# Kernel optimization log

Hardware: AMD Instinct MI355X
Metric: run time of the kernel (lower is better)

## Reference

```python
import jax, jax.numpy as jnp
import numpy as np

NUM_NODES = 5  # the 5 ASPP branches form the graph nodes


def conv2d(x, w, b, padding=0, dilation=1):
    # NCHW conv with OIHW kernel, stride 1
    out = jax.lax.conv_general_dilated(
        x, w, window_strides=(1, 1),
        padding=[(padding, padding), (padding, padding)],
        rhs_dilation=(dilation, dilation),
        dimension_numbers=("NCHW", "OIHW", "NCHW"))
    return out + b[None, :, None, None]


def setup_inputs() -> dict:
    key = jax.random.key(0)
    ks = jax.random.split(key, 16)
    Cin, Cmid, Cout = 32, 16, 32
    B, H, W = 8, 384, 384
    s = 0.05
    inp = {
        "x": jax.random.normal(ks[0], (B, Cin, H, W), jnp.float32),
        "w1": jax.random.normal(ks[1], (Cmid, Cin, 1, 1), jnp.float32) * s,
        "b1": jax.random.normal(ks[2], (Cmid,), jnp.float32) * s,
        "w2": jax.random.normal(ks[3], (Cmid, Cin, 3, 3), jnp.float32) * s,
        "b2": jax.random.normal(ks[4], (Cmid,), jnp.float32) * s,
        "w3": jax.random.normal(ks[5], (Cmid, Cin, 3, 3), jnp.float32) * s,
        "b3": jax.random.normal(ks[6], (Cmid,), jnp.float32) * s,
        "w4": jax.random.normal(ks[7], (Cmid, Cin, 3, 3), jnp.float32) * s,
        "b4": jax.random.normal(ks[8], (Cmid,), jnp.float32) * s,
        "w5": jax.random.normal(ks[9], (Cmid, Cin, 1, 1), jnp.float32) * s,
        "b5": jax.random.normal(ks[10], (Cmid,), jnp.float32) * s,
        "gcn_w": jax.random.normal(ks[11], (Cmid, Cmid), jnp.float32) * s,
        "gcn_b": jax.random.normal(ks[12], (Cmid,), jnp.float32) * s,
        "attn_weights": jnp.ones((NUM_NODES,), jnp.float32),
        "fusion_w": jax.random.normal(ks[13], (Cout, Cmid, 1, 1), jnp.float32) * s,
        "fusion_b": jax.random.normal(ks[14], (Cout,), jnp.float32) * s,
    }
    return inp


def reference(x, w1, b1, w2, b2, w3, b3, w4, b4, w5, b5,
              gcn_w, gcn_b, attn_weights, fusion_w, fusion_b):
    # --- ASPP branches ---
    f1 = conv2d(x, w1, b1)                     # 1x1
    f2 = conv2d(x, w2, b2, padding=1, dilation=1)
    f3 = conv2d(x, w3, b3, padding=2, dilation=2)
    f4 = conv2d(x, w4, b4, padding=3, dilation=3)
    gap = x.mean(axis=(2, 3), keepdims=True)   # AdaptiveAvgPool2d(1)
    f5 = conv2d(gap, w5, b5)                   # [B, mid, 1, 1]
    # bilinear upsample of a 1x1 map (align_corners=False) == broadcast
    f5 = jnp.broadcast_to(f5, f1.shape)
    feats = jnp.stack([f1, f2, f3, f4, f5], axis=1)  # [B, 5, mid, H, W]

    # --- node features: per-branch global mean ---
    node_feats = feats.mean(axis=(3, 4))       # [B, 5, mid]

    # --- GCNConv on complete 5-node graph (self-loops added by GCNConv):
    # A_hat = D^{-1/2}(A+I)D^{-1/2} = ones(5,5)/5. Batched over samples.
    A_hat = jnp.full((NUM_NODES, NUM_NODES), 1.0 / NUM_NODES, dtype=x.dtype)
    fused_nodes = jnp.einsum("ij,bjc->bic", A_hat, node_feats @ gcn_w) + gcn_b  # [B,5,mid]

    # --- weighted node fusion ---
    weights = jax.nn.softmax(attn_weights)     # [5]
    out = jnp.einsum("i,bichw,bic->bchw", weights, feats, fused_nodes)  # [B, mid, H, W]

    return conv2d(out, fusion_w, fusion_b)     # [B, out, H, W]
```

## Files before the change

kernel.cpp:

```cpp
#include <hip/hip_runtime.h>
#include <math.h>

#define HH 384
#define WW 384
#define BB 8
#define CIN 32
#define CMID 16
#define COUT 32
#define HWP (HH*WW)

#define WS_GAP  0
#define WS_BORD 256
#define WS_F5   12544
#define WS_CB   12672
#define WS_W2   12928
#define WS_WBF  17024
#define WS_S    32768

typedef __attribute__((ext_vector_type(8))) __bf16 bf16x8;
typedef __attribute__((ext_vector_type(4))) float  f32x4;

__device__ __forceinline__ unsigned bf16r(float f) {
    unsigned u = __float_as_uint(f);
    return (u + 0x7fffu + ((u >> 16) & 1u)) >> 16;
}

__device__ __forceinline__ void softmax5(const float* attn, float sw[5]) {
    float a0=attn[0],a1=attn[1],a2=attn[2],a3=attn[3],a4=attn[4];
    float m = fmaxf(fmaxf(fmaxf(a0,a1),fmaxf(a2,a3)),a4);
    float e0=expf(a0-m),e1=expf(a1-m),e2=expf(a2-m),e3=expf(a3-m),e4=expf(a4-m);
    float inv = 1.f/(e0+e1+e2+e3+e4);
    sw[0]=e0*inv; sw[1]=e1*inv; sw[2]=e2*inv; sw[3]=e3*inv; sw[4]=e4*inv;
}

__global__ void gap_kernel(const float* __restrict__ x, float* __restrict__ gap) {
    int plane = blockIdx.x;
    const float4* xp = (const float4*)(x + (size_t)plane * HWP);
    float s = 0.f;
    for (int i = threadIdx.x; i < HWP/4; i += 1024) {
        float4 v = xp[i];
        s += (v.x + v.y) + (v.z + v.w);
    }
    __shared__ float red[16];
    #pragma unroll
    for (int o = 32; o; o >>= 1) s += __shfl_down(s, o);
    if ((threadIdx.x & 63) == 0) red[threadIdx.x >> 6] = s;
    __syncthreads();
    if (threadIdx.x < 16) {
        float t = red[threadIdx.x];
        #pragma unroll
        for (int o = 8; o; o >>= 1) t += __shfl_down(t, o);
        if (threadIdx.x == 0) gap[plane] = t * (1.f / (float)HWP);
    }
}

__device__ __forceinline__ float blockReduce256(float v, float* red) {
    #pragma unroll
    for (int o = 32; o; o >>= 1) v += __shfl_down(v, o);
    if ((threadIdx.x & 63) == 0) red[threadIdx.x >> 6] = v;
    __syncthreads();
    float r = 0.f;
    if (threadIdx.x == 0) r = red[0] + red[1] + red[2] + red[3];
    __syncthreads();
    return r;
}

__global__ void border_kernel(const float* __restrict__ x, float* __restrict__ bord) {
    int plane = blockIdx.x;
    const float* xp = x + (size_t)plane * HWP;
    __shared__ float red[4];
    __shared__ float rs[6], cs[6];
    int t = threadIdx.x;
    for (int j = 0; j < 6; ++j) {
        int r = (j < 3) ? j : 378 + j;
        float s = 0.f;
        for (int i = t; i < WW; i += 256) s += xp[r*WW + i];
        s = blockReduce256(s, red);
        if (t == 0) rs[j] = s;
    }
    for (int j = 0; j < 6; ++j) {
        int c = (j < 3) ? j : 378 + j;
        float s = 0.f;
        for (int i = t; i < HH; i += 256) s += xp[i*WW + c];
        s = blockReduce256(s, red);
        if (t == 0) cs[j] = s;
    }
    __syncthreads();
    if (t == 0) {
        float* bd = bord + plane*48;
        bd[0]=rs[0]; bd[1]=rs[0]+rs[1]; bd[2]=rs[0]+rs[1]+rs[2];
        bd[3]=rs[5]; bd[4]=rs[5]+rs[4]; bd[5]=rs[5]+rs[4]+rs[3];
        bd[6]=cs[0]; bd[7]=cs[0]+cs[1]; bd[8]=cs[0]+cs[1]+cs[2];
        bd[9]=cs[5]; bd[10]=cs[5]+cs[4]; bd[11]=cs[5]+cs[4]+cs[3];
        for (int a = 1; a <= 3; ++a)
        for (int b2 = 1; b2 <= 3; ++b2) {
            float tl=0,tr=0,bl=0,br=0;
            for (int h = 0; h < a; ++h)
            for (int w = 0; w < b2; ++w) {
                tl += xp[h*WW + w];
                tr += xp[h*WW + (WW-1-w)];
                bl += xp[(HH-1-h)*WW + w];
                br += xp[(HH-1-h)*WW + (WW-1-w)];
            }
            int o = (a-1)*3 + (b2-1);
            bd[12+o]=tl; bd[21+o]=tr; bd[30+o]=bl; bd[39+o]=br;
        }
    }
}

__global__ void prep1_kernel(const float* __restrict__ w1, const float* __restrict__ w2,
                             const float* __restrict__ w3, const float* __restrict__ w4,
                             const float* __restrict__ w5, const float* __restrict__ b5,
                             const float* __restrict__ attn, float* __restrict__ ws) {
    const float* gap = ws + WS_GAP;
    float* f5 = ws + WS_F5;
    unsigned short* wbf = (unsigned short*)(ws + WS_WBF);
    float sw[5];
    softmax5(attn, sw);
    int t = threadIdx.x;
    if (t < 128) {
        int b = t >> 4, c = t & 15;
        float acc = b5[c];
        for (int ci = 0; ci < CIN; ++ci) acc += w5[c*CIN+ci] * gap[b*CIN+ci];
        f5[t] = acc;
    }
    const int tk[8] = {0,1,2,3,5,6,7,8};
    for (int idx = t; idx < 25*512; idx += blockDim.x) {
        int tap  = idx >> 9;
        int lane = (idx >> 3) & 63;
        int j    = idx & 7;
        int cin  = ((lane >> 4) << 3) | j;
        int c    = lane & 15;
        float v;
        if (tap == 0) {
            v = sw[0]*w1[c*CIN+cin]
              + sw[1]*w2[c*288 + cin*9 + 4]
              + sw[2]*w3[c*288 + cin*9 + 4]
              + sw[3]*w4[c*288 + cin*9 + 4];
        } else {
            int g = (tap-1) >> 3;
            int m = (tap-1) & 7;
            int kk = tk[m];
            const float* w = (g == 0) ? w2 : ((g == 1) ? w3 : w4);
            v = sw[g+1] * w[c*288 + cin*9 + kk];
        }
        wbf[idx] = (unsigned short)bf16r(v);
    }
}

__global__ __launch_bounds__(256) void conv_kernel(
        const float* __restrict__ x, const unsigned short* __restrict__ wBf,
        float* __restrict__ S) {
    __shared__ __align__(16) unsigned short sx[484*40];
    int blk = blockIdx.x;
    int b = blk / 576; int tno = blk % 576;
    int h0 = (tno / 24) * 16, w0 = (tno % 24) * 16;
    int tid = threadIdx.x;

    int i0 = tid, i1 = tid + 256;
    int r0i = i0 / 22, c0i = i0 - r0i*22;
    int r1i = i1 / 22, c1i = i1 - r1i*22;
    int gh0 = h0 - 3 + r0i, gw0 = w0 - 3 + c0i;
    int gh1 = h0 - 3 + r1i, gw1 = w0 - 3 + c1i;
    bool ok0 = ((unsigned)gh0 < (unsigned)HH) && ((unsigned)gw0 < (unsigned)WW);
    bool ok1 = ((unsigned)gh1 < (unsigned)HH) && ((unsigned)gw1 < (unsigned)WW) && (i1 < 484);
    bool has1 = (i1 < 484);
    int go0 = ok0 ? (gh0*WW + gw0) : 0;
    int go1 = ok1 ? (gh1*WW + gw1) : 0;
    unsigned* sxu = (unsigned*)sx;
    const float* xb = x + (size_t)b * CIN * HWP;
    #pragma unroll 4
    for (int cp = 0; cp < 16; ++cp) {
        const float* p0 = xb + (size_t)(2*cp) * HWP;
        const float* p1 = p0 + HWP;
        float a0 = ok0 ? p0[go0] : 0.f;
        float a1 = ok0 ? p1[go0] : 0.f;
        sxu[i0*20 + cp] = bf16r(a0) | (bf16r(a1) << 16);
        if (has1) {
            float d0 = ok1 ? p0[go1] : 0.f;
            float d1 = ok1 ? p1[go1] : 0.f;
            sxu[i1*20 + cp] = bf16r(d0) | (bf16r(d1) << 16);
        }
    }
    __syncthreads();

    int lane = tid & 63, wv = tid >> 6;
    int m = lane & 15, q = lane >> 4;
    int by0 = ((wv*4 + 0 + 3)*22 + 3 + m)*40 + q*8;
    int by1 = by0 + 22*40;
    int by2 = by1 + 22*40;
    int by3 = by2 + 22*40;
    const unsigned short* wfp = wBf + lane*8;

    f32x4 acc0 = {0.f,0.f,0.f,0.f}, acc1 = {0.f,0.f,0.f,0.f};
    f32x4 acc2 = {0.f,0.f,0.f,0.f}, acc3 = {0.f,0.f,0.f,0.f};

    constexpr int TDH[25] = {0, -1,-1,-1,0,0,1,1,1, -2,-2,-2,0,0,2,2,2, -3,-3,-3,0,0,3,3,3};
    constexpr int TDW[25] = {0, -1,0,1,-1,1,-1,0,1, -2,0,2,-2,2,-2,0,2, -3,0,3,-3,3,-3,0,3};
    #pragma unroll
    for (int tap = 0; tap < 25; ++tap) {
        bf16x8 bw = *(const bf16x8*)(wfp + tap*512);
        const int to = (TDH[tap]*22 + TDW[tap])*40;
        acc0 = __builtin_amdgcn_mfma_f32_16x16x32_bf16(*(const bf16x8*)(sx + by0 + to), bw, acc0, 0, 0, 0);
        acc1 = __builtin_amdgcn_mfma_f32_16x16x32_bf16(*(const bf16x8*)(sx + by1 + to), bw, acc1, 0, 0, 0);
        acc2 = __builtin_amdgcn_mfma_f32_16x16x32_bf16(*(const bf16x8*)(sx + by2 + to), bw, acc2, 0, 0, 0);
        acc3 = __builtin_amdgcn_mfma_f32_16x16x32_bf16(*(const bf16x8*)(sx + by3 + to), bw, acc3, 0, 0, 0);
    }

    #pragma unroll
    for (int g2 = 0; g2 < 4; ++g2) {
        int y = wv*4 + g2;
        float* sp = S + ((size_t)b*HWP + (size_t)(h0 + y)*WW + w0) * 16;
        f32x4 a = (g2 == 0) ? acc0 : (g2 == 1) ? acc1 : (g2 == 2) ? acc2 : acc3;
        #pragma unroll
        for (int r = 0; r < 4; ++r) {
            int px = q*4 + r;
            sp[px*16 + m] = a[r];
        }
    }
}

__device__ __forceinline__ float rectsum(const float* bd, float T, int dh, int dw) {
    int r0 = dh > 0 ?  dh : 0, b0 = dh < 0 ? -dh : 0;
    int c0 = dw > 0 ?  dw : 0, d0 = dw < 0 ? -dw : 0;
    float v = T;
    if (r0) v -= bd[r0-1];
    if (b0) v -= bd[3+b0-1];
    if (c0) v -= bd[6+c0-1];
    if (d0) v -= bd[9+d0-1];
    if (r0 && c0) v += bd[12+(r0-1)*3+(c0-1)];
    if (r0 && d0) v += bd[21+(r0-1)*3+(d0-1)];
    if (b0 && c0) v += bd[30+(b0-1)*3+(c0-1)];
    if (b0 && d0) v += bd[39+(b0-1)*3+(d0-1)];
    return v;
}

__global__ void prep2_kernel(const float* __restrict__ w1,
                             const float* __restrict__ b1, const float* __restrict__ w2,
                             const float* __restrict__ b2, const float* __restrict__ w3,
                             const float* __restrict__ b3, const float* __restrict__ w4,
                             const float* __restrict__ b4,
                             const float* __restrict__ gcn_w, const float* __restrict__ gcn_b,
                             const float* __restrict__ fusion_w, const float* __restrict__ fusion_b,
                             const float* __restrict__ attn, float* __restrict__ ws) {
    const float* gap  = ws + WS_GAP;
    const float* bord = ws + WS_BORD;
    const float* f5   = ws + WS_F5;
    float* W2 = ws + WS_W2;
    float* CB = ws + WS_CB;
    __shared__ float ns[128];
    __shared__ float bbf[128];
    __shared__ float gl[128];
    float sw[5];
    softmax5(attn, sw);
    int t = threadIdx.x;
    const float invHW = 1.f / (float)HWP;
    if (t < 128) {
        int b = t >> 4, c = t & 15;
        float nf1 = b1[c];
        float s2 = 0.f, s3 = 0.f, s4 = 0.f;
        for (int cin = 0; cin < CIN; ++cin) {
            nf1 += w1[c*CIN+cin] * gap[b*CIN+cin];
            const float* bd = bord + (b*CIN + cin)*48;
            float T = gap[b*CIN+cin] * (float)HWP;
            #pragma unroll
            for (int kk = 0; kk < 9; ++kk) {
                int dh = (kk/3) - 1, dw = (kk%3) - 1;
                float wv2 = w2[c*288 + cin*9 + kk];
                float wv3 = w3[c*288 + cin*9 + kk];
                float wv4 = w4[c*288 + cin*9 + kk];
                s2 += wv2 * rectsum(bd, T, dh,   dw);
                s3 += wv3 * rectsum(bd, T, 2*dh, 2*dw);
                s4 += wv4 * rectsum(bd, T, 3*dh, 3*dw);
            }
        }
        float nf2 = b2[c] + s2*invHW;
        float nf3 = b3[c] + s3*invHW;
        float nf4 = b4[c] + s4*invHW;
        float nf5 = f5[b*16 + c];
        ns[t]  = 0.2f * (nf1 + nf2 + nf3 + nf4 + nf5);
        bbf[t] = sw[0]*b1[c] + sw[1]*b2[c] + sw[2]*b3[c] + sw[3]*b4[c] + sw[4]*nf5;
    }
    __syncthreads();
    if (t < 128) {
        int b = t >> 4, c = t & 15;
        float acc = gcn_b[c];
        for (int k = 0; k < 16; ++k) acc += ns[b*16 + k] * gcn_w[k*16 + c];
        gl[t] = acc;
    }
    __syncthreads();
    for (int idx = t; idx < 4096; idx += blockDim.x) {
        int b = idx >> 9, c = (idx >> 5) & 15, co = idx & 31;
        W2[idx] = fusion_w[co*16 + c] * gl[b*16 + c];
    }
    if (t < 256) {
        int b = t >> 5, co = t & 31;
        float acc = fusion_b[co];
        for (int c = 0; c < 16; ++c)
            acc += fusion_w[co*16 + c] * gl[b*16 + c] * bbf[b*16 + c];
        CB[t] = acc;
    }
}

__global__ __launch_bounds__(256) void fuse_kernel(const float* __restrict__ ws_ro,
                                                   float* __restrict__ out) {
    __shared__ float w2s[512];
    __shared__ float cbs[32];
    int blk = blockIdx.x;
    int b = blk / 576;
    int pl = (blk % 576) * 256 + threadIdx.x;
    int t = threadIdx.x;
    const float* W2 = ws_ro + WS_W2 + b*512;
    w2s[t] = W2[t];
    w2s[t + 256] = W2[t + 256];
    if (t < 32) cbs[t] = ws_ro[WS_CB + b*32 + t];
    __syncthreads();

    const float4* sp = (const float4*)(ws_ro + WS_S + ((size_t)b*HWP + pl)*16);
    float4 s0 = sp[0], s1 = sp[1], s2 = sp[2], s3 = sp[3];
    float sv[16] = {s0.x,s0.y,s0.z,s0.w, s1.x,s1.y,s1.z,s1.w,
                    s2.x,s2.y,s2.z,s2.w, s3.x,s3.y,s3.z,s3.w};
    float acc[32];
    #pragma unroll
    for (int co = 0; co < 32; ++co) acc[co] = cbs[co];
    #pragma unroll
    for (int c = 0; c < 16; ++c) {
        float v = sv[c];
        #pragma unroll
        for (int co = 0; co < 32; ++co) acc[co] = fmaf(w2s[c*32 + co], v, acc[co]);
    }
    float* ob = out + (size_t)b * COUT * HWP + pl;
    #pragma unroll
    for (int co = 0; co < 32; ++co) ob[(size_t)co * HWP] = acc[co];
}

extern "C" void kernel_launch(void* const* d_in, const int* in_sizes, int n_in,
                              void* d_out, int out_size, void* d_ws, size_t ws_size,
                              hipStream_t stream) {
    const float* x     = (const float*)d_in[0];
    const float* w1    = (const float*)d_in[1];  const float* b1 = (const float*)d_in[2];
    const float* w2    = (const float*)d_in[3];  const float* b2 = (const float*)d_in[4];
    const float* w3    = (const float*)d_in[5];  const float* b3 = (const float*)d_in[6];
    const float* w4    = (const float*)d_in[7];  const float* b4 = (const float*)d_in[8];
    const float* w5    = (const float*)d_in[9];  const float* b5 = (const float*)d_in[10];
    const float* gcn_w = (const float*)d_in[11]; const float* gcn_b = (const float*)d_in[12];
    const float* attn  = (const float*)d_in[13];
    const float* fw    = (const float*)d_in[14]; const float* fb = (const float*)d_in[15];
    float* ws  = (float*)d_ws;
    float* out = (float*)d_out;

    gap_kernel   <<<256, 1024, 0, stream>>>(x, ws + WS_GAP);
    border_kernel<<<256, 256, 0, stream>>>(x, ws + WS_BORD);
    prep1_kernel <<<1, 256, 0, stream>>>(w1, w2, w3, w4, w5, b5, attn, ws);
    conv_kernel  <<<4608, 256, 0, stream>>>(x, (const unsigned short*)(ws + WS_WBF), ws + WS_S);
    prep2_kernel <<<1, 256, 0, stream>>>(w1, b1, w2, b2, w3, b3, w4, b4,
                                         gcn_w, gcn_b, fw, fb, attn, ws);
    fuse_kernel  <<<4608, 256, 0, stream>>>(ws, out);
}
```

Before: 485.1 us.

## Fuse conv and fusion stages, precompute NHWC bf16 input with fused reductions

Adds a transform pass that reads x once, writes a channel-last bf16 copy, and in the same pass accumulates global sums and border row/column sums with atomics. This replaces the separate gap and border kernels. The conv kernel now loads contiguous bf16 pixel vectors, and the per-pixel 16→32 fusion projection is fused into it through shared memory, so the fp32 intermediate S buffer is never written or read back. The added cost is an extra write and read of a bf16 copy of x, plus atomics and a memset.

```diff
diff --git a/kernel.cpp b/kernel.cpp
--- a/kernel.cpp
+++ b/kernel.cpp
@@ -3,19 +3,16 @@
 
 #define HH 384
 #define WW 384
-#define BB 8
 #define CIN 32
-#define CMID 16
-#define COUT 32
 #define HWP (HH*WW)
 
-#define WS_GAP  0
-#define WS_BORD 256
-#define WS_F5   12544
-#define WS_CB   12672
-#define WS_W2   12928
-#define WS_WBF  17024
-#define WS_S    32768
+#define WS_GSUM 0
+#define WS_ROWS 256
+#define WS_COLS 1792
+#define WS_W2   3328
+#define WS_CB   7424
+#define WS_WBF  7680
+#define WS_XBF  16384
 
 typedef __attribute__((ext_vector_type(8))) __bf16 bf16x8;
 typedef __attribute__((ext_vector_type(4))) float  f32x4;
@@ -33,190 +30,46 @@
     sw[0]=e0*inv; sw[1]=e1*inv; sw[2]=e2*inv; sw[3]=e3*inv; sw[4]=e4*inv;
 }
 
-__global__ void gap_kernel(const float* __restrict__ x, float* __restrict__ gap) {
-    int plane = blockIdx.x;
-    const float4* xp = (const float4*)(x + (size_t)plane * HWP);
-    float s = 0.f;
-    for (int i = threadIdx.x; i < HWP/4; i += 1024) {
-        float4 v = xp[i];
-        s += (v.x + v.y) + (v.z + v.w);
-    }
-    __shared__ float red[16];
-    #pragma unroll
-    for (int o = 32; o; o >>= 1) s += __shfl_down(s, o);
-    if ((threadIdx.x & 63) == 0) red[threadIdx.x >> 6] = s;
-    __syncthreads();
-    if (threadIdx.x < 16) {
-        float t = red[threadIdx.x];
+__global__ __launch_bounds__(384) void transform_kernel(const float* __restrict__ x,
+        float* __restrict__ ws, unsigned short* __restrict__ xbf) {
+    int b = blockIdx.x / HH, h = blockIdx.x % HH;
+    int t = threadIdx.x;
+    const float* xp = x + (size_t)b*CIN*HWP + (size_t)h*WW + t;
+    float v[32];
+    #pragma unroll
+    for (int ci = 0; ci < 32; ++ci) v[ci] = xp[(size_t)ci*HWP];
+
+    unsigned uu[16];
+    #pragma unroll
+    for (int k = 0; k < 16; ++k) uu[k] = bf16r(v[2*k]) | (bf16r(v[2*k+1]) << 16);
+    uint4* dst = (uint4*)(xbf + ((size_t)b*HWP + (size_t)h*WW + t)*32);
+    dst[0] = make_uint4(uu[0],uu[1],uu[2],uu[3]);
+    dst[1] = make_uint4(uu[4],uu[5],uu[6],uu[7]);
+    dst[2] = make_uint4(uu[8],uu[9],uu[10],uu[11]);
+    dst[3] = make_uint4(uu[12],uu[13],uu[14],uu[15]);
+
+    int cj = (t < 3) ? t : ((t >= 381) ? t - 378 : -1);
+    if (cj >= 0) {
         #pragma unroll
-        for (int o = 8; o; o >>= 1) t += __shfl_down(t, o);
-        if (threadIdx.x == 0) gap[plane] = t * (1.f / (float)HWP);
-    }
-}
-
-__device__ __forceinline__ float blockReduce256(float v, float* red) {
-    #pragma unroll
-    for (int o = 32; o; o >>= 1) v += __shfl_down(v, o);
-    if ((threadIdx.x & 63) == 0) red[threadIdx.x >> 6] = v;
-    __syncthreads();
-    float r = 0.f;
-    if (threadIdx.x == 0) r = red[0] + red[1] + red[2] + red[3];
-    __syncthreads();
-    return r;
-}
-
-__global__ void border_kernel(const float* __restrict__ x, float* __restrict__ bord) {
-    int plane = blockIdx.x;
-    const float* xp = x + (size_t)plane * HWP;
-    __shared__ float red[4];
-    __shared__ float rs[6], cs[6];
-    int t = threadIdx.x;
-    for (int j = 0; j < 6; ++j) {
-        int r = (j < 3) ? j : 378 + j;
-        float s = 0.f;
-        for (int i = t; i < WW; i += 256) s += xp[r*WW + i];
-        s = blockReduce256(s, red);
-        if (t == 0) rs[j] = s;
-    }
-    for (int j = 0; j < 6; ++j) {
-        int c = (j < 3) ? j : 378 + j;
-        float s = 0.f;
-        for (int i = t; i < HH; i += 256) s += xp[i*WW + c];
-        s = blockReduce256(s, red);
-        if (t == 0) cs[j] = s;
-    }
-    __syncthreads();
-    if (t == 0) {
-        float* bd = bord + plane*48;
-        bd[0]=rs[0]; bd[1]=rs[0]+rs[1]; bd[2]=rs[0]+rs[1]+rs[2];
-        bd[3]=rs[5]; bd[4]=rs[5]+rs[4]; bd[5]=rs[5]+rs[4]+rs[3];
-        bd[6]=cs[0]; bd[7]=cs[0]+cs[1]; bd[8]=cs[0]+cs[1]+cs[2];
-        bd[9]=cs[5]; bd[10]=cs[5]+cs[4]; bd[11]=cs[5]+cs[4]+cs[3];
-        for (int a = 1; a <= 3; ++a)
-        for (int b2 = 1; b2 <= 3; ++b2) {
-            float tl=0,tr=0,bl=0,br=0;
-            for (int h = 0; h < a; ++h)
-            for (int w = 0; w < b2; ++w) {
-                tl += xp[h*WW + w];
-                tr += xp[h*WW + (WW-1-w)];
-                bl += xp[(HH-1-h)*WW + w];
-                br += xp[(HH-1-h)*WW + (WW-1-w)];
-            }
-            int o = (a-1)*3 + (b2-1);
-            bd[12+o]=tl; bd[21+o]=tr; bd[30+o]=bl; bd[39+o]=br;
-        }
-    }
-}
-
-__global__ void prep1_kernel(const float* __restrict__ w1, const float* __restrict__ w2,
-                             const float* __restrict__ w3, const float* __restrict__ w4,
-                             const float* __restrict__ w5, const float* __restrict__ b5,
-                             const float* __restrict__ attn, float* __restrict__ ws) {
-    const float* gap = ws + WS_GAP;
-    float* f5 = ws + WS_F5;
-    unsigned short* wbf = (unsigned short*)(ws + WS_WBF);
-    float sw[5];
-    softmax5(attn, sw);
-    int t = threadIdx.x;
-    if (t < 128) {
-        int b = t >> 4, c = t & 15;
-        float acc = b5[c];
-        for (int ci = 0; ci < CIN; ++ci) acc += w5[c*CIN+ci] * gap[b*CIN+ci];
-        f5[t] = acc;
-    }
-    const int tk[8] = {0,1,2,3,5,6,7,8};
-    for (int idx = t; idx < 25*512; idx += blockDim.x) {
-        int tap  = idx >> 9;
-        int lane = (idx >> 3) & 63;
-        int j    = idx & 7;
-        int cin  = ((lane >> 4) << 3) | j;
-        int c    = lane & 15;
-        float v;
-        if (tap == 0) {
-            v = sw[0]*w1[c*CIN+cin]
-              + sw[1]*w2[c*288 + cin*9 + 4]
-              + sw[2]*w3[c*288 + cin*9 + 4]
-              + sw[3]*w4[c*288 + cin*9 + 4];
-        } else {
-            int g = (tap-1) >> 3;
-            int m = (tap-1) & 7;
-            int kk = tk[m];
-            const float* w = (g == 0) ? w2 : ((g == 1) ? w3 : w4);
-            v = sw[g+1] * w[c*288 + cin*9 + kk];
-        }
-        wbf[idx] = (unsigned short)bf16r(v);
-    }
-}
-
-__global__ __launch_bounds__(256) void conv_kernel(
-        const float* __restrict__ x, const unsigned short* __restrict__ wBf,
-        float* __restrict__ S) {
-    __shared__ __align__(16) unsigned short sx[484*40];
-    int blk = blockIdx.x;
-    int b = blk / 576; int tno = blk % 576;
-    int h0 = (tno / 24) * 16, w0 = (tno % 24) * 16;
-    int tid = threadIdx.x;
-
-    int i0 = tid, i1 = tid + 256;
-    int r0i = i0 / 22, c0i = i0 - r0i*22;
-    int r1i = i1 / 22, c1i = i1 - r1i*22;
-    int gh0 = h0 - 3 + r0i, gw0 = w0 - 3 + c0i;
-    int gh1 = h0 - 3 + r1i, gw1 = w0 - 3 + c1i;
-    bool ok0 = ((unsigned)gh0 < (unsigned)HH) && ((unsigned)gw0 < (unsigned)WW);
-    bool ok1 = ((unsigned)gh1 < (unsigned)HH) && ((unsigned)gw1 < (unsigned)WW) && (i1 < 484);
-    bool has1 = (i1 < 484);
-    int go0 = ok0 ? (gh0*WW + gw0) : 0;
-    int go1 = ok1 ? (gh1*WW + gw1) : 0;
-    unsigned* sxu = (unsigned*)sx;
-    const float* xb = x + (size_t)b * CIN * HWP;
-    #pragma unroll 4
-    for (int cp = 0; cp < 16; ++cp) {
-        const float* p0 = xb + (size_t)(2*cp) * HWP;
-        const float* p1 = p0 + HWP;
-        float a0 = ok0 ? p0[go0] : 0.f;
-        float a1 = ok0 ? p1[go0] : 0.f;
-        sxu[i0*20 + cp] = bf16r(a0) | (bf16r(a1) << 16);
-        if (has1) {
-            float d0 = ok1 ? p0[go1] : 0.f;
-            float d1 = ok1 ? p1[go1] : 0.f;
-            sxu[i1*20 + cp] = bf16r(d0) | (bf16r(d1) << 16);
-        }
-    }
-    __syncthreads();
-
-    int lane = tid & 63, wv = tid >> 6;
-    int m = lane & 15, q = lane >> 4;
-    int by0 = ((wv*4 + 0 + 3)*22 + 3 + m)*40 + q*8;
-    int by1 = by0 + 22*40;
-    int by2 = by1 + 22*40;
-    int by3 = by2 + 22*40;
-    const unsigned short* wfp = wBf + lane*8;
-
-    f32x4 acc0 = {0.f,0.f,0.f,0.f}, acc1 = {0.f,0.f,0.f,0.f};
-    f32x4 acc2 = {0.f,0.f,0.f,0.f}, acc3 = {0.f,0.f,0.f,0.f};
-
-    constexpr int TDH[25] = {0, -1,-1,-1,0,0,1,1,1, -2,-2,-2,0,0,2,2,2, -3,-3,-3,0,0,3,3,3};
-    constexpr int TDW[25] = {0, -1,0,1,-1,1,-1,0,1, -2,0,2,-2,2,-2,0,2, -3,0,3,-3,3,-3,0,3};
-    #pragma unroll
-    for (int tap = 0; tap < 25; ++tap) {
-        bf16x8 bw = *(const bf16x8*)(wfp + tap*512);
-        const int to = (TDH[tap]*22 + TDW[tap])*40;
-        acc0 = __builtin_amdgcn_mfma_f32_16x16x32_bf16(*(const bf16x8*)(sx + by0 + to), bw, acc0, 0, 0, 0);
-        acc1 = __builtin_amdgcn_mfma_f32_16x16x32_bf16(*(const bf16x8*)(sx + by1 + to), bw, acc1, 0, 0, 0);
-        acc2 = __builtin_amdgcn_mfma_f32_16x16x32_bf16(*(const bf16x8*)(sx + by2 + to), bw, acc2, 0, 0, 0);
-        acc3 = __builtin_amdgcn_mfma_f32_16x16x32_bf16(*(const bf16x8*)(sx + by3 + to), bw, acc3, 0, 0, 0);
-    }
-
-    #pragma unroll
-    for (int g2 = 0; g2 < 4; ++g2) {
-        int y = wv*4 + g2;
-        float* sp = S + ((size_t)b*HWP + (size_t)(h0 + y)*WW + w0) * 16;
-        f32x4 a = (g2 == 0) ? acc0 : (g2 == 1) ? acc1 : (g2 == 2) ? acc2 : acc3;
+        for (int ci = 0; ci < 32; ++ci)
+            atomicAdd(&ws[WS_COLS + (b*32 + ci)*6 + cj], v[ci]);
+    }
+
+    __shared__ float red[32][6];
+    int wv = t >> 6, ln = t & 63;
+    #pragma unroll
+    for (int ci = 0; ci < 32; ++ci) {
+        float s = v[ci];
         #pragma unroll
-        for (int r = 0; r < 4; ++r) {
-            int px = q*4 + r;
-            sp[px*16 + m] = a[r];
-        }
+        for (int o = 32; o; o >>= 1) s += __shfl_down(s, o);
+        if (ln == 0) red[ci][wv] = s;
+    }
+    __syncthreads();
+    if (t < 32) {
+        float rsum = red[t][0]+red[t][1]+red[t][2]+red[t][3]+red[t][4]+red[t][5];
+        atomicAdd(&ws[WS_GSUM + b*32 + t], rsum);
+        int rj = (h < 3) ? h : ((h >= 381) ? h - 378 : -1);
+        if (rj >= 0) ws[WS_ROWS + (b*32 + t)*6 + rj] = rsum;
     }
 }
 
@@ -235,51 +88,103 @@
     return v;
 }
 
-__global__ void prep2_kernel(const float* __restrict__ w1,
-                             const float* __restrict__ b1, const float* __restrict__ w2,
-                             const float* __restrict__ b2, const float* __restrict__ w3,
-                             const float* __restrict__ b3, const float* __restrict__ w4,
-                             const float* __restrict__ b4,
-                             const float* __restrict__ gcn_w, const float* __restrict__ gcn_b,
-                             const float* __restrict__ fusion_w, const float* __restrict__ fusion_b,
-                             const float* __restrict__ attn, float* __restrict__ ws) {
-    const float* gap  = ws + WS_GAP;
-    const float* bord = ws + WS_BORD;
-    const float* f5   = ws + WS_F5;
-    float* W2 = ws + WS_W2;
-    float* CB = ws + WS_CB;
-    __shared__ float ns[128];
-    __shared__ float bbf[128];
-    __shared__ float gl[128];
+__global__ void prep_kernel(const float* __restrict__ x,
+                            const float* __restrict__ w1, const float* __restrict__ b1,
+                            const float* __restrict__ w2, const float* __restrict__ b2,
+                            const float* __restrict__ w3, const float* __restrict__ b3,
+                            const float* __restrict__ w4, const float* __restrict__ b4,
+                            const float* __restrict__ w5, const float* __restrict__ b5,
+                            const float* __restrict__ gcn_w, const float* __restrict__ gcn_b,
+                            const float* __restrict__ fusion_w, const float* __restrict__ fusion_b,
+                            const float* __restrict__ attn, float* __restrict__ ws) {
+    __shared__ float sbd[256*48];
+    __shared__ float ns[128], bbf[128], gl[128];
     float sw[5];
     softmax5(attn, sw);
     int t = threadIdx.x;
     const float invHW = 1.f / (float)HWP;
+
+    {
+        int plane = t;
+        float* bd = sbd + plane*48;
+        const float* rw = ws + WS_ROWS + plane*6;
+        const float* cl = ws + WS_COLS + plane*6;
+        bd[0]=rw[0]; bd[1]=rw[0]+rw[1]; bd[2]=rw[0]+rw[1]+rw[2];
+        bd[3]=rw[5]; bd[4]=rw[5]+rw[4]; bd[5]=rw[5]+rw[4]+rw[3];
+        bd[6]=cl[0]; bd[7]=cl[0]+cl[1]; bd[8]=cl[0]+cl[1]+cl[2];
+        bd[9]=cl[5]; bd[10]=cl[5]+cl[4]; bd[11]=cl[5]+cl[4]+cl[3];
+        const float* xp = x + (size_t)plane*HWP;
+        for (int a = 1; a <= 3; ++a)
+        for (int b2 = 1; b2 <= 3; ++b2) {
+            float tl=0,tr=0,bl=0,br=0;
+            for (int h = 0; h < a; ++h)
+            for (int w = 0; w < b2; ++w) {
+                tl += xp[h*WW + w];
+                tr += xp[h*WW + (WW-1-w)];
+                bl += xp[(HH-1-h)*WW + w];
+                br += xp[(HH-1-h)*WW + (WW-1-w)];
+            }
+            int o = (a-1)*3 + (b2-1);
+            bd[12+o]=tl; bd[21+o]=tr; bd[30+o]=bl; bd[39+o]=br;
+        }
+    }
+
+    float f5v = 0.f;
+    if (t < 128) {
+        int b = t >> 4, c = t & 15;
+        f5v = b5[c];
+        for (int ci = 0; ci < CIN; ++ci)
+            f5v += w5[c*CIN+ci] * ws[WS_GSUM + b*32 + ci] * invHW;
+    }
+    {
+        unsigned short* wbf = (unsigned short*)(ws + WS_WBF);
+        const int tk[8] = {0,1,2,3,5,6,7,8};
+        for (int idx = t; idx < 25*512; idx += blockDim.x) {
+            int tap  = idx >> 9;
+            int lane = (idx >> 3) & 63;
+            int j    = idx & 7;
+            int cin  = ((lane >> 4) << 3) | j;
+            int c    = lane & 15;
+            float v;
+            if (tap == 0) {
+                v = sw[0]*w1[c*CIN+cin]
+                  + sw[1]*w2[c*288 + cin*9 + 4]
+                  + sw[2]*w3[c*288 + cin*9 + 4]
+                  + sw[3]*w4[c*288 + cin*9 + 4];
+            } else {
+                int g = (tap-1) >> 3;
+                int mth = (tap-1) & 7;
+                int kk = tk[mth];
+                const float* w = (g == 0) ? w2 : ((g == 1) ? w3 : w4);
+                v = sw[g+1] * w[c*288 + cin*9 + kk];
+            }
+            wbf[idx] = (unsigned short)bf16r(v);
+        }
+    }
+    __syncthreads();
+
     if (t < 128) {
         int b = t >> 4, c = t & 15;
         float nf1 = b1[c];
         float s2 = 0.f, s3 = 0.f, s4 = 0.f;
         for (int cin = 0; cin < CIN; ++cin) {
-            nf1 += w1[c*CIN+cin] * gap[b*CIN+cin];
-            const float* bd = bord + (b*CIN + cin)*48;
-            float T = gap[b*CIN+cin] * (float)HWP;
+            int plane = b*32 + cin;
+            float T = ws[WS_GSUM + plane];
+            nf1 += w1[c*CIN+cin] * T * invHW;
+            const float* bd = sbd + plane*48;
             #pragma unroll
             for (int kk = 0; kk < 9; ++kk) {
                 int dh = (kk/3) - 1, dw = (kk%3) - 1;
-                float wv2 = w2[c*288 + cin*9 + kk];
-                float wv3 = w3[c*288 + cin*9 + kk];
-                float wv4 = w4[c*288 + cin*9 + kk];
-                s2 += wv2 * rectsum(bd, T, dh,   dw);
-                s3 += wv3 * rectsum(bd, T, 2*dh, 2*dw);
-                s4 += wv4 * rectsum(bd, T, 3*dh, 3*dw);
+                s2 += w2[c*288 + cin*9 + kk] * rectsum(bd, T, dh,   dw);
+                s3 += w3[c*288 + cin*9 + kk] * rectsum(bd, T, 2*dh, 2*dw);
+                s4 += w4[c*288 + cin*9 + kk] * rectsum(bd, T, 3*dh, 3*dw);
             }
         }
         float nf2 = b2[c] + s2*invHW;
         float nf3 = b3[c] + s3*invHW;
         float nf4 = b4[c] + s4*invHW;
-        float nf5 = f5[b*16 + c];
-        ns[t]  = 0.2f * (nf1 + nf2 + nf3 + nf4 + nf5);
-        bbf[t] = sw[0]*b1[c] + sw[1]*b2[c] + sw[2]*b3[c] + sw[3]*b4[c] + sw[4]*nf5;
+        ns[t]  = 0.2f * (nf1 + nf2 + nf3 + nf4 + f5v);
+        bbf[t] = sw[0]*b1[c] + sw[1]*b2[c] + sw[2]*b3[c] + sw[3]*b4[c] + sw[4]*f5v;
     }
     __syncthreads();
     if (t < 128) {
@@ -291,35 +196,86 @@
     __syncthreads();
     for (int idx = t; idx < 4096; idx += blockDim.x) {
         int b = idx >> 9, c = (idx >> 5) & 15, co = idx & 31;
-        W2[idx] = fusion_w[co*16 + c] * gl[b*16 + c];
-    }
-    if (t < 256) {
+        ws[WS_W2 + idx] = fusion_w[co*16 + c] * gl[b*16 + c];
+    }
+    {
         int b = t >> 5, co = t & 31;
         float acc = fusion_b[co];
         for (int c = 0; c < 16; ++c)
             acc += fusion_w[co*16 + c] * gl[b*16 + c] * bbf[b*16 + c];
-        CB[t] = acc;
-    }
-}
-
-__global__ __launch_bounds__(256) void fuse_kernel(const float* __restrict__ ws_ro,
-                                                   float* __restrict__ out) {
-    __shared__ float w2s[512];
-    __shared__ float cbs[32];
+        ws[WS_CB + t] = acc;
+    }
+}
+
+__global__ __launch_bounds__(256) void convfuse_kernel(
+        const unsigned short* __restrict__ xbf, const unsigned short* __restrict__ wBf,
+        const float* __restrict__ ws_ro, float* __restrict__ out) {
+    __shared__ __align__(16) char smem[40896];
+    unsigned short* sx = (unsigned short*)smem;
+    float* w2s = (float*)(smem + 38720);
+    float* cbs = (float*)(smem + 40768);
     int blk = blockIdx.x;
-    int b = blk / 576;
-    int pl = (blk % 576) * 256 + threadIdx.x;
-    int t = threadIdx.x;
-    const float* W2 = ws_ro + WS_W2 + b*512;
-    w2s[t] = W2[t];
-    w2s[t + 256] = W2[t + 256];
-    if (t < 32) cbs[t] = ws_ro[WS_CB + b*32 + t];
-    __syncthreads();
-
-    const float4* sp = (const float4*)(ws_ro + WS_S + ((size_t)b*HWP + pl)*16);
-    float4 s0 = sp[0], s1 = sp[1], s2 = sp[2], s3 = sp[3];
-    float sv[16] = {s0.x,s0.y,s0.z,s0.w, s1.x,s1.y,s1.z,s1.w,
-                    s2.x,s2.y,s2.z,s2.w, s3.x,s3.y,s3.z,s3.w};
+    int b = blk / 576, tno = blk % 576;
+    int h0 = (tno / 24) * 16, w0 = (tno % 24) * 16;
+    int tid = threadIdx.x;
+
+    w2s[tid]       = ws_ro[WS_W2 + b*512 + tid];
+    w2s[tid + 256] = ws_ro[WS_W2 + b*512 + 256 + tid];
+    if (tid < 32) cbs[tid] = ws_ro[WS_CB + b*32 + tid];
+
+    for (int p = tid; p < 484; p += 256) {
+        int r = p / 22, c = p - r*22;
+        int gh = h0 - 3 + r, gw = w0 - 3 + c;
+        uint4 a0 = {0,0,0,0}, a1 = a0, a2 = a0, a3 = a0;
+        if ((unsigned)gh < (unsigned)HH && (unsigned)gw < (unsigned)WW) {
+            const uint4* src = (const uint4*)(xbf + ((size_t)b*HWP + (size_t)gh*WW + gw)*32);
+            a0 = src[0]; a1 = src[1]; a2 = src[2]; a3 = src[3];
+        }
+        uint4* d = (uint4*)(sx + p*40);
+        d[0] = a0; d[1] = a1; d[2] = a2; d[3] = a3;
+    }
+    __syncthreads();
+
+    int lane = tid & 63, wv = tid >> 6;
+    int m = lane & 15, q = lane >> 4;
+    int by0 = ((wv*4 + 0 + 3)*22 + 3 + m)*40 + q*8;
+    int by1 = by0 + 22*40;
+    int by2 = by1 + 22*40;
+    int by3 = by2 + 22*40;
+    const unsigned short* wfp = wBf + lane*8;
+
+    f32x4 acc0 = {0.f,0.f,0.f,0.f}, acc1 = {0.f,0.f,0.f,0.f};
+    f32x4 acc2 = {0.f,0.f,0.f,0.f}, acc3 = {0.f,0.f,0.f,0.f};
+
+    constexpr int TDH[25] = {0, -1,-1,-1,0,0,1,1,1, -2,-2,-2,0,0,2,2,2, -3,-3,-3,0,0,3,3,3};
+    constexpr int TDW[25] = {0, -1,0,1,-1,1,-1,0,1, -2,0,2,-2,2,-2,0,2, -3,0,3,-3,3,-3,0,3};
+    #pragma unroll
+    for (int tap = 0; tap < 25; ++tap) {
+        bf16x8 bw = *(const bf16x8*)(wfp + tap*512);
+        const int to = (TDH[tap]*22 + TDW[tap])*40;
+        acc0 = __builtin_amdgcn_mfma_f32_16x16x32_bf16(*(const bf16x8*)(sx + by0 + to), bw, acc0, 0, 0, 0);
+        acc1 = __builtin_amdgcn_mfma_f32_16x16x32_bf16(*(const bf16x8*)(sx + by1 + to), bw, acc1, 0, 0, 0);
+        acc2 = __builtin_amdgcn_mfma_f32_16x16x32_bf16(*(const bf16x8*)(sx + by2 + to), bw, acc2, 0, 0, 0);
+        acc3 = __builtin_amdgcn_mfma_f32_16x16x32_bf16(*(const bf16x8*)(sx + by3 + to), bw, acc3, 0, 0, 0);
+    }
+    __syncthreads();
+
+    float* st = (float*)smem;
+    #pragma unroll
+    for (int g2 = 0; g2 < 4; ++g2) {
+        int y = wv*4 + g2;
+        f32x4 a = (g2 == 0) ? acc0 : (g2 == 1) ? acc1 : (g2 == 2) ? acc2 : acc3;
+        #pragma unroll
+        for (int r = 0; r < 4; ++r) {
+            int px = q*4 + r;
+            st[(y*16 + px)*17 + m] = a[r];
+        }
+    }
+    __syncthreads();
+
+    float sv[16];
+    #pragma unroll
+    for (int c = 0; c < 16; ++c) sv[c] = st[tid*17 + c];
     float acc[32];
     #pragma unroll
     for (int co = 0; co < 32; ++co) acc[co] = cbs[co];
@@ -329,7 +285,8 @@
         #pragma unroll
         for (int co = 0; co < 32; ++co) acc[co] = fmaf(w2s[c*32 + co], v, acc[co]);
     }
-    float* ob = out + (size_t)b * COUT * HWP + pl;
+    int y = tid >> 4, px = tid & 15;
+    float* ob = out + (size_t)b*32*HWP + (size_t)(h0 + y)*WW + w0 + px;
     #pragma unroll
     for (int co = 0; co < 32; ++co) ob[(size_t)co * HWP] = acc[co];
 }
@@ -348,12 +305,11 @@
     const float* fw    = (const float*)d_in[14]; const float* fb = (const float*)d_in[15];
     float* ws  = (float*)d_ws;
     float* out = (float*)d_out;
-
-    gap_kernel   <<<256, 1024, 0, stream>>>(x, ws + WS_GAP);
-    border_kernel<<<256, 256, 0, stream>>>(x, ws + WS_BORD);
-    prep1_kernel <<<1, 256, 0, stream>>>(w1, w2, w3, w4, w5, b5, attn, ws);
-    conv_kernel  <<<4608, 256, 0, stream>>>(x, (const unsigned short*)(ws + WS_WBF), ws + WS_S);
-    prep2_kernel <<<1, 256, 0, stream>>>(w1, b1, w2, b2, w3, b3, w4, b4,
-                                         gcn_w, gcn_b, fw, fb, attn, ws);
-    fuse_kernel  <<<4608, 256, 0, stream>>>(ws, out);
-}
+    unsigned short* xbf = (unsigned short*)(ws + WS_XBF);
+
+    hipMemsetAsync(ws, 0, 3328 * sizeof(float), stream);
+    transform_kernel<<<8*HH, 384, 0, stream>>>(x, ws, xbf);
+    prep_kernel     <<<1, 256, 0, stream>>>(x, w1,b1,w2,b2,w3,b3,w4,b4,w5,b5,
+                                            gcn_w, gcn_b, fw, fb, attn, ws);
+    convfuse_kernel <<<4608, 256, 0, stream>>>(xbf, (const unsigned short*)(ws + WS_WBF), ws, out);
+}
```

Measured after the change: 481.3 us. Within noise of the previous version (-0.8%).
